# Optimization experiments

Hardware: AMD Instinct MI355X
Metric: run time of the kernel (lower is better)

The kernel has to match this reference:

```python
import jax, jax.numpy as jnp
import numpy as np

N, C_IN, C_OUT = 8192, 128, 128
BN_EPS = 1e-5
EDGE_PROB = 0.004  # avg degree ~33


def setup_inputs() -> dict:
    key = jax.random.key(0)
    k1, k2, k3, k4, k5, k6 = jax.random.split(key, 6)
    node_features = jax.random.normal(k1, (N, C_IN), dtype=jnp.float32)
    # binary dense adjacency (rand fill, thresholded to ~avg degree 33)
    adjacency_matrix = (jax.random.uniform(k2, (N, N)) < EDGE_PROB).astype(jnp.float32)
    s = 1.0 / np.sqrt(C_IN)
    W_n = jax.random.uniform(k3, (C_OUT, C_IN), jnp.float32, -s, s)
    b_n = jax.random.uniform(k4, (C_OUT,), jnp.float32, -s, s)
    W_c = jax.random.uniform(k5, (C_OUT, C_IN), jnp.float32, -s, s)
    b_c = jax.random.uniform(k6, (C_OUT,), jnp.float32, -s, s)
    gamma = jnp.ones((C_OUT,), jnp.float32)
    beta = jnp.zeros((C_OUT,), jnp.float32)
    return {"node_features": node_features, "adjacency_matrix": adjacency_matrix,
            "W_n": W_n, "b_n": b_n, "W_c": W_c, "b_c": b_c,
            "gamma": gamma, "beta": beta}


def reference(node_features, adjacency_matrix, W_n, b_n, W_c, b_c, gamma, beta):
    # mean aggregation: degrees from row-sums (as in the torch code), agg = A.T @ X / deg
    deg = adjacency_matrix.sum(axis=1, keepdims=True)          # [N,1]
    deg = jnp.where(deg == 0, jnp.ones_like(deg), deg)
    agg = (adjacency_matrix.T @ node_features) / deg           # [N,C_in]
    h = agg @ W_n.T + b_n + node_features @ W_c.T + b_c        # [N,C_out]
    # BatchNorm1d, training-mode batch stats (biased variance)
    mu = h.mean(axis=0)
    var = ((h - mu) ** 2).mean(axis=0)
    h_norm = (h - mu) * jax.lax.rsqrt(var + BN_EPS)
    return jax.nn.relu(gamma * h_norm + beta)
```

## Files before the change

### kernel.cpp

```cpp
#include <hip/hip_runtime.h>
#include <stdint.h>

#define NN 8192
#define CC 128
#define BN_EPS 1e-5f

__device__ inline unsigned short f2bf(float f) {
    unsigned int u = __float_as_uint(f);
    unsigned int r = (u + 0x7fffu + ((u >> 16) & 1u)) >> 16;
    return (unsigned short)r;
}
__device__ inline float bf2f(unsigned short s) {
    return __uint_as_float(((unsigned int)s) << 16);
}

__device__ __forceinline__ void process_pair(
        float4 a, float xa0, float xb0, float xa1, float xb1,
        int j0, float* __restrict__ acc, float* __restrict__ deg, int lane) {
    unsigned long long m0 = __ballot(a.x != 0.0f);
    unsigned long long m1 = __ballot(a.y != 0.0f);
    unsigned long long m2 = __ballot(a.z != 0.0f);
    unsigned long long m3 = __ballot(a.w != 0.0f);
    if ((m0 | m1 | m2 | m3) == 0ull) return;
    const unsigned long long LO = 0xffffffffull;
    int c0 = __popcll(m0 & LO) + __popcll(m1 & LO) + __popcll(m2 & LO) + __popcll(m3 & LO);
    int c1 = __popcll(m0 >> 32) + __popcll(m1 >> 32) + __popcll(m2 >> 32) + __popcll(m3 >> 32);
    if (lane == 0 && c0) atomicAdd(&deg[j0], (float)c0);
    if (lane == 1 && c1) atomicAdd(&deg[j0 + 1], (float)c1);
    unsigned long long m[4] = {m0, m1, m2, m3};
    #pragma unroll
    for (int comp = 0; comp < 4; ++comp) {
        unsigned int lo = (unsigned int)m[comp];
        while (lo) {
            int b = __builtin_ctz(lo); lo &= lo - 1;
            int il = 4 * b + comp;
            atomicAdd(&acc[il * 128 + lane],      xa0);
            atomicAdd(&acc[il * 128 + 64 + lane], xb0);
        }
        unsigned int hi = (unsigned int)(m[comp] >> 32);
        while (hi) {
            int b = __builtin_ctz(hi); hi &= hi - 1;
            int il = 4 * b + comp;
            atomicAdd(&acc[il * 128 + lane],      xa1);
            atomicAdd(&acc[il * 128 + 64 + lane], xb1);
        }
    }
}

#define LOADB(a_, xa_, xb_, j0_) do {                                          \
    const float* Ap_ = A + (size_t)((j0_) + (lane >> 5)) * NN + i0 + ((lane & 31) << 2); \
    _Pragma("unroll")                                                          \
    for (int u = 0; u < 4; ++u)                                                \
        a_[u] = *reinterpret_cast<const float4*>(Ap_ + (size_t)(2 * u) * NN);  \
    _Pragma("unroll")                                                          \
    for (int r = 0; r < 8; ++r) {                                              \
        xa_[r] = X[((j0_) + r) * CC + lane];                                   \
        xb_[r] = X[((j0_) + r) * CC + 64 + lane];                              \
    }                                                                          \
} while (0)

#define PROCB(a_, xa_, xb_, j0_) do {                                          \
    _Pragma("unroll")                                                          \
    for (int u = 0; u < 4; ++u)                                                \
        process_pair(a_[u], xa_[2 * u], xb_[2 * u], xa_[2 * u + 1],            \
                     xb_[2 * u + 1], (j0_) + 2 * u, acc, deg, lane);           \
} while (0)

__global__ __launch_bounds__(256, 2) void k1_spmm(
        const float* __restrict__ A, const float* __restrict__ X,
        float* __restrict__ aggU, float* __restrict__ deg) {
    __shared__ float acc[128 * 128];
    const int tid  = threadIdx.x;
    const int lane = tid & 63;
    const int wave = tid >> 6;
    const int i0   = blockIdx.x * 128;
    const int jbase = blockIdx.y * 1024 + wave * 256;

    for (int t = tid; t < 128 * 128; t += 256) acc[t] = 0.0f;
    __syncthreads();

    float4 a0[4], a1[4];
    float xa0[8], xb0[8], xa1[8], xb1[8];

    LOADB(a0, xa0, xb0, jbase);
    for (int it2 = 0; it2 < 16; ++it2) {
        int j0 = jbase + it2 * 16;
        LOADB(a1, xa1, xb1, j0 + 8);
        PROCB(a0, xa0, xb0, j0);
        if (it2 < 15) LOADB(a0, xa0, xb0, j0 + 16);
        PROCB(a1, xa1, xb1, j0 + 8);
    }

    __syncthreads();
    float* aggBase = aggU + (size_t)i0 * CC;
    for (int t = tid; t < 128 * 128; t += 256) atomicAdd(&aggBase[t], acc[t]);
}

__global__ __launch_bounds__(256, 2) void k2_gemm(
        const float* __restrict__ aggU, const float* __restrict__ deg,
        const float* __restrict__ X,
        const float* __restrict__ Wn, const float* __restrict__ bn,
        const float* __restrict__ Wc, const float* __restrict__ bc,
        float* __restrict__ h, float* __restrict__ bsum, float* __restrict__ bsq) {
    __shared__ unsigned short WtN[128 * 128];
    __shared__ unsigned short WtC[128 * 128];
    const int tid = threadIdx.x;
    for (int idx = tid * 4; idx < 128 * 128; idx += 1024) {
        float4 wn4 = *reinterpret_cast<const float4*>(Wn + idx);
        float4 wc4 = *reinterpret_cast<const float4*>(Wc + idx);
        int c = idx >> 7, k0 = idx & 127;
        WtN[(k0 + 0) * 128 + c] = f2bf(wn4.x);
        WtN[(k0 + 1) * 128 + c] = f2bf(wn4.y);
        WtN[(k0 + 2) * 128 + c] = f2bf(wn4.z);
        WtN[(k0 + 3) * 128 + c] = f2bf(wn4.w);
        WtC[(k0 + 0) * 128 + c] = f2bf(wc4.x);
        WtC[(k0 + 1) * 128 + c] = f2bf(wc4.y);
        WtC[(k0 + 2) * 128 + c] = f2bf(wc4.z);
        WtC[(k0 + 3) * 128 + c] = f2bf(wc4.w);
    }
    __syncthreads();
    const int c  = tid & 127;
    const int rg = tid >> 7;
    const int i0 = blockIdx.x * 16 + rg * 8;

    float accN[8], accC[8];
    #pragma unroll
    for (int r = 0; r < 8; ++r) { accN[r] = 0.0f; accC[r] = 0.0f; }

    float4 ar[8], xr[8], an[8], xn[8];

#define LOADK(ab_, xb_, k_) do {                                               \
    _Pragma("unroll")                                                          \
    for (int r = 0; r < 8; ++r) {                                              \
        ab_[r] = *reinterpret_cast<const float4*>(&aggU[(size_t)(i0 + r) * CC + (k_)]); \
        xb_[r] = *reinterpret_cast<const float4*>(&X[(size_t)(i0 + r) * CC + (k_)]);    \
    }                                                                          \
} while (0)

#define COMPK(ab_, xb_, k_) do {                                               \
    _Pragma("unroll")                                                          \
    for (int kk = 0; kk < 4; ++kk) {                                           \
        float wn_ = bf2f(WtN[((k_) + kk) * 128 + c]);                          \
        float wc_ = bf2f(WtC[((k_) + kk) * 128 + c]);                          \
        _Pragma("unroll")                                                      \
        for (int r = 0; r < 8; ++r) {                                          \
            accN[r] = fmaf((&ab_[r].x)[kk], wn_, accN[r]);                     \
            accC[r] = fmaf((&xb_[r].x)[kk], wc_, accC[r]);                     \
        }                                                                      \
    }                                                                          \
} while (0)

    LOADK(ar, xr, 0);
    for (int k = 0; k < 128; k += 8) {
        LOADK(an, xn, k + 4);
        COMPK(ar, xr, k);
        if (k + 8 < 128) LOADK(ar, xr, k + 8);
        COMPK(an, xn, k + 4);
    }

    const float bnc = bn[c], bcc = bc[c];
    float sp = 0.0f, sq = 0.0f;
    #pragma unroll
    for (int r = 0; r < 8; ++r) {
        float d  = deg[i0 + r];
        float rd = (d == 0.0f) ? 1.0f : (1.0f / d);
        float hv = accN[r] * rd + accC[r] + bnc + bcc;
        h[(size_t)(i0 + r) * CC + c] = hv;
        sp += hv; sq += hv * hv;
    }
    __syncthreads();
    float* red = reinterpret_cast<float*>(WtN);
    red[rg * 128 + c]       = sp;
    red[256 + rg * 128 + c] = sq;
    __syncthreads();
    if (rg == 0) {
        atomicAdd(&bsum[c], red[c] + red[128 + c]);
        atomicAdd(&bsq[c],  red[256 + c] + red[384 + c]);
    }
}

__global__ __launch_bounds__(256) void k4_bn(
        const float* __restrict__ h, const float* __restrict__ bsum,
        const float* __restrict__ bsq, const float* __restrict__ gamma,
        const float* __restrict__ beta, float* __restrict__ out) {
    const int idx = (blockIdx.x * 256 + threadIdx.x) * 4;
    const int c0  = idx & 127;
    float4 hv = *reinterpret_cast<const float4*>(h + idx);
    float4 s4 = *reinterpret_cast<const float4*>(bsum + c0);
    float4 q4 = *reinterpret_cast<const float4*>(bsq + c0);
    float4 g4 = *reinterpret_cast<const float4*>(gamma + c0);
    float4 b4 = *reinterpret_cast<const float4*>(beta + c0);
    const float invN = 1.0f / 8192.0f;
    float4 o;
    const float* hp = &hv.x; const float* sp = &s4.x; const float* qp = &q4.x;
    const float* gp = &g4.x; const float* bp = &b4.x; float* op = &o.x;
    #pragma unroll
    for (int jj = 0; jj < 4; ++jj) {
        float mu  = sp[jj] * invN;
        float var = qp[jj] * invN - mu * mu;
        float sc  = gp[jj] * rsqrtf(var + BN_EPS);
        float v   = (hp[jj] - mu) * sc + bp[jj];
        op[jj] = v > 0.0f ? v : 0.0f;
    }
    *reinterpret_cast<float4*>(out + idx) = o;
}

extern "C" void kernel_launch(void* const* d_in, const int* in_sizes, int n_in,
                              void* d_out, int out_size, void* d_ws, size_t ws_size,
                              hipStream_t stream) {
    const float* X     = (const float*)d_in[0];
    const float* A     = (const float*)d_in[1];
    const float* Wn    = (const float*)d_in[2];
    const float* bn    = (const float*)d_in[3];
    const float* Wc    = (const float*)d_in[4];
    const float* bc    = (const float*)d_in[5];
    const float* gamma = (const float*)d_in[6];
    const float* beta  = (const float*)d_in[7];
    float* out = (float*)d_out;

    char* ws = (char*)d_ws;
    float* aggU = (float*)(ws);
    float* deg  = (float*)(ws + 4194304);
    float* bsum = (float*)(ws + 4227072);
    float* bsq  = (float*)(ws + 4227584);
    float* h    = (float*)(ws + 4228096);

    hipMemsetAsync(d_ws, 0, 4228096, stream);

    k1_spmm<<<dim3(64, 8), 256, 0, stream>>>(A, X, aggU, deg);
    k2_gemm<<<512, 256, 0, stream>>>(aggU, deg, X, Wn, bn, Wc, bc, h, bsum, bsq);
    k4_bn<<<1024, 256, 0, stream>>>(h, bsum, bsq, gamma, beta, out);
}
```

Measured before the change: 531.9 us.

## Compress adjacency to bitmasks, then gather neighbor features per node

Replaces the shared-memory atomic scatter SpMM with two kernels. The first streams the dense adjacency once, builds transposed 64-bit nonzero masks and row degrees with ballots. The second has one wave per output node walk the set bits and accumulate neighbor feature rows in registers, applying the degree normalization there instead of in the GEMM. This removes the per-nonzero LDS atomics and the global atomic flush of the partial aggregates, at the cost of an extra 8 MB mask buffer and irregular gathers of X.

```diff
diff --git a/kernel.cpp b/kernel.cpp
--- a/kernel.cpp
+++ b/kernel.cpp
@@ -14,91 +14,78 @@
     return __uint_as_float(((unsigned int)s) << 16);
 }
 
-__device__ __forceinline__ void process_pair(
-        float4 a, float xa0, float xb0, float xa1, float xb1,
-        int j0, float* __restrict__ acc, float* __restrict__ deg, int lane) {
-    unsigned long long m0 = __ballot(a.x != 0.0f);
-    unsigned long long m1 = __ballot(a.y != 0.0f);
-    unsigned long long m2 = __ballot(a.z != 0.0f);
-    unsigned long long m3 = __ballot(a.w != 0.0f);
-    if ((m0 | m1 | m2 | m3) == 0ull) return;
-    const unsigned long long LO = 0xffffffffull;
-    int c0 = __popcll(m0 & LO) + __popcll(m1 & LO) + __popcll(m2 & LO) + __popcll(m3 & LO);
-    int c1 = __popcll(m0 >> 32) + __popcll(m1 >> 32) + __popcll(m2 >> 32) + __popcll(m3 >> 32);
-    if (lane == 0 && c0) atomicAdd(&deg[j0], (float)c0);
-    if (lane == 1 && c1) atomicAdd(&deg[j0 + 1], (float)c1);
-    unsigned long long m[4] = {m0, m1, m2, m3};
-    #pragma unroll
-    for (int comp = 0; comp < 4; ++comp) {
-        unsigned int lo = (unsigned int)m[comp];
-        while (lo) {
-            int b = __builtin_ctz(lo); lo &= lo - 1;
-            int il = 4 * b + comp;
-            atomicAdd(&acc[il * 128 + lane],      xa0);
-            atomicAdd(&acc[il * 128 + 64 + lane], xb0);
+__global__ __launch_bounds__(256) void k1a_mask(
+        const float* __restrict__ A, unsigned long long* __restrict__ Mt,
+        float* __restrict__ deg) {
+    const int lane = threadIdx.x & 63;
+    const int task = blockIdx.x * 4 + (threadIdx.x >> 6);
+    const int band = task >> 5;
+    const int i0   = (task & 31) << 8;
+    const int j0   = band << 6;
+
+    const float4* Ap = reinterpret_cast<const float4*>(A + (size_t)j0 * NN + i0) + lane;
+    unsigned long long m0 = 0, m1 = 0, m2 = 0, m3 = 0;
+    int degc = 0;
+
+    #pragma unroll 8
+    for (int j = 0; j < 64; ++j) {
+        float4 v = Ap[(size_t)j * (NN / 4)];
+        bool n0 = v.x != 0.0f, n1 = v.y != 0.0f, n2 = v.z != 0.0f, n3 = v.w != 0.0f;
+        unsigned long long b0 = __ballot(n0), b1 = __ballot(n1);
+        unsigned long long b2 = __ballot(n2), b3 = __ballot(n3);
+        const unsigned long long bit = 1ull << j;
+        if (n0) m0 |= bit;
+        if (n1) m1 |= bit;
+        if (n2) m2 |= bit;
+        if (n3) m3 |= bit;
+        int cnt = __popcll(b0) + __popcll(b1) + __popcll(b2) + __popcll(b3);
+        if (lane == j) degc = cnt;
+    }
+
+    atomicAdd(&deg[j0 + lane], (float)degc);
+    unsigned long long* p = Mt + (size_t)band * NN + i0 + 4 * lane;
+    reinterpret_cast<ulonglong2*>(p)[0] = make_ulonglong2(m0, m1);
+    reinterpret_cast<ulonglong2*>(p)[1] = make_ulonglong2(m2, m3);
+}
+
+__global__ __launch_bounds__(256) void k1c_gather(
+        const unsigned long long* __restrict__ Mt, const float* __restrict__ X,
+        const float* __restrict__ deg, float* __restrict__ aggN) {
+    const int lane = threadIdx.x & 63;
+    const int i = blockIdx.x * 4 + (threadIdx.x >> 6);
+
+    unsigned long long w0 = Mt[(size_t)(2 * lane) * NN + i];
+    unsigned long long w1 = Mt[(size_t)(2 * lane + 1) * NN + i];
+    float acc0 = 0.0f, acc1 = 0.0f;
+
+    unsigned long long any = __ballot((w0 | w1) != 0ull);
+    while (any) {
+        int q = __builtin_ctzll(any); any &= any - 1;
+        unsigned long long u0 = __shfl(w0, q);
+        unsigned long long u1 = __shfl(w1, q);
+        const float* Xq = X + (size_t)q * 128 * CC;
+        while (u0) {
+            int b = __builtin_ctzll(u0); u0 &= u0 - 1;
+            const float* xr = Xq + b * CC;
+            acc0 += xr[lane];
+            acc1 += xr[64 + lane];
         }
-        unsigned int hi = (unsigned int)(m[comp] >> 32);
-        while (hi) {
-            int b = __builtin_ctz(hi); hi &= hi - 1;
-            int il = 4 * b + comp;
-            atomicAdd(&acc[il * 128 + lane],      xa1);
-            atomicAdd(&acc[il * 128 + 64 + lane], xb1);
+        while (u1) {
+            int b = __builtin_ctzll(u1); u1 &= u1 - 1;
+            const float* xr = Xq + (b + 64) * CC;
+            acc0 += xr[lane];
+            acc1 += xr[64 + lane];
         }
     }
-}
-
-#define LOADB(a_, xa_, xb_, j0_) do {                                          \
-    const float* Ap_ = A + (size_t)((j0_) + (lane >> 5)) * NN + i0 + ((lane & 31) << 2); \
-    _Pragma("unroll")                                                          \
-    for (int u = 0; u < 4; ++u)                                                \
-        a_[u] = *reinterpret_cast<const float4*>(Ap_ + (size_t)(2 * u) * NN);  \
-    _Pragma("unroll")                                                          \
-    for (int r = 0; r < 8; ++r) {                                              \
-        xa_[r] = X[((j0_) + r) * CC + lane];                                   \
-        xb_[r] = X[((j0_) + r) * CC + 64 + lane];                              \
-    }                                                                          \
-} while (0)
-
-#define PROCB(a_, xa_, xb_, j0_) do {                                          \
-    _Pragma("unroll")                                                          \
-    for (int u = 0; u < 4; ++u)                                                \
-        process_pair(a_[u], xa_[2 * u], xb_[2 * u], xa_[2 * u + 1],            \
-                     xb_[2 * u + 1], (j0_) + 2 * u, acc, deg, lane);           \
-} while (0)
-
-__global__ __launch_bounds__(256, 2) void k1_spmm(
-        const float* __restrict__ A, const float* __restrict__ X,
-        float* __restrict__ aggU, float* __restrict__ deg) {
-    __shared__ float acc[128 * 128];
-    const int tid  = threadIdx.x;
-    const int lane = tid & 63;
-    const int wave = tid >> 6;
-    const int i0   = blockIdx.x * 128;
-    const int jbase = blockIdx.y * 1024 + wave * 256;
-
-    for (int t = tid; t < 128 * 128; t += 256) acc[t] = 0.0f;
-    __syncthreads();
-
-    float4 a0[4], a1[4];
-    float xa0[8], xb0[8], xa1[8], xb1[8];
-
-    LOADB(a0, xa0, xb0, jbase);
-    for (int it2 = 0; it2 < 16; ++it2) {
-        int j0 = jbase + it2 * 16;
-        LOADB(a1, xa1, xb1, j0 + 8);
-        PROCB(a0, xa0, xb0, j0);
-        if (it2 < 15) LOADB(a0, xa0, xb0, j0 + 16);
-        PROCB(a1, xa1, xb1, j0 + 8);
-    }
-
-    __syncthreads();
-    float* aggBase = aggU + (size_t)i0 * CC;
-    for (int t = tid; t < 128 * 128; t += 256) atomicAdd(&aggBase[t], acc[t]);
+
+    float d  = deg[i];
+    float rd = (d == 0.0f) ? 1.0f : (1.0f / d);
+    aggN[(size_t)i * CC + lane]      = acc0 * rd;
+    aggN[(size_t)i * CC + 64 + lane] = acc1 * rd;
 }
 
 __global__ __launch_bounds__(256, 2) void k2_gemm(
-        const float* __restrict__ aggU, const float* __restrict__ deg,
-        const float* __restrict__ X,
+        const float* __restrict__ aggN, const float* __restrict__ X,
         const float* __restrict__ Wn, const float* __restrict__ bn,
         const float* __restrict__ Wc, const float* __restrict__ bc,
         float* __restrict__ h, float* __restrict__ bsum, float* __restrict__ bsq) {
@@ -132,7 +119,7 @@
 #define LOADK(ab_, xb_, k_) do {                                               \
     _Pragma("unroll")                                                          \
     for (int r = 0; r < 8; ++r) {                                              \
-        ab_[r] = *reinterpret_cast<const float4*>(&aggU[(size_t)(i0 + r) * CC + (k_)]); \
+        ab_[r] = *reinterpret_cast<const float4*>(&aggN[(size_t)(i0 + r) * CC + (k_)]); \
         xb_[r] = *reinterpret_cast<const float4*>(&X[(size_t)(i0 + r) * CC + (k_)]);    \
     }                                                                          \
 } while (0)
@@ -162,9 +149,7 @@
     float sp = 0.0f, sq = 0.0f;
     #pragma unroll
     for (int r = 0; r < 8; ++r) {
-        float d  = deg[i0 + r];
-        float rd = (d == 0.0f) ? 1.0f : (1.0f / d);
-        float hv = accN[r] * rd + accC[r] + bnc + bcc;
+        float hv = accN[r] + accC[r] + bnc + bcc;
         h[(size_t)(i0 + r) * CC + c] = hv;
         sp += hv; sq += hv * hv;
     }
@@ -219,15 +204,17 @@
     float* out = (float*)d_out;
 
     char* ws = (char*)d_ws;
-    float* aggU = (float*)(ws);
-    float* deg  = (float*)(ws + 4194304);
-    float* bsum = (float*)(ws + 4227072);
-    float* bsq  = (float*)(ws + 4227584);
-    float* h    = (float*)(ws + 4228096);
-
-    hipMemsetAsync(d_ws, 0, 4228096, stream);
-
-    k1_spmm<<<dim3(64, 8), 256, 0, stream>>>(A, X, aggU, deg);
-    k2_gemm<<<512, 256, 0, stream>>>(aggU, deg, X, Wn, bn, Wc, bc, h, bsum, bsq);
-    k4_bn<<<1024, 256, 0, stream>>>(h, bsum, bsq, gamma, beta, out);
-}
+    float* deg  = (float*)(ws);
+    float* bsum = (float*)(ws + 32768);
+    float* bsq  = (float*)(ws + 33280);
+    float* aggN = (float*)(ws + 65536);
+    unsigned long long* Mt = (unsigned long long*)(ws + 4259840);
+    float* h    = (float*)(ws + 4259840);
+
+    hipMemsetAsync(d_ws, 0, 33792, stream);
+
+    k1a_mask  <<<1024, 256, 0, stream>>>(A, Mt, deg);
+    k1c_gather<<<2048, 256, 0, stream>>>(Mt, X, deg, aggN);
+    k2_gemm   <<<512,  256, 0, stream>>>(aggN, X, Wn, bn, Wc, bc, h, bsum, bsq);
+    k4_bn     <<<1024, 256, 0, stream>>>(h, bsum, bsq, gamma, beta, out);
+}
```

Result: faster. 464.7 us (-12.6%).
